# Kernel tuning notes

Hardware: AMD Instinct MI355X
Metric: run time of the kernel (lower is better)

## Reference

```python
import jax, jax.numpy as jnp
import numpy as np

NUM_HEADS = 16


def setup_inputs() -> dict:
    key = jax.random.key(0)
    k1, k2, k3 = jax.random.split(key, 3)
    b, s, d_model = 4, 4096, 1024
    x = jax.random.normal(k1, (b, s, d_model), dtype=jnp.float32)
    w_qkv = jax.random.normal(k2, (3 * d_model, d_model), dtype=jnp.float32) * 0.02
    b_qkv = jnp.zeros((3 * d_model,), dtype=jnp.float32)
    w_out = jax.random.normal(k3, (d_model, d_model), dtype=jnp.float32) * 0.02
    b_out = jnp.zeros((d_model,), dtype=jnp.float32)
    return {"x": x, "w_qkv": w_qkv, "b_qkv": b_qkv, "w_out": w_out, "b_out": b_out}


def reference(x, w_qkv, b_qkv, w_out, b_out):
    b, s, d_model = x.shape
    h = NUM_HEADS
    hd = d_model // h
    # qkv projection: [b, s, 3*d_model]
    qkv = jnp.einsum('bsd,ed->bse', x, w_qkv) + b_qkv
    # rearrange 'b s (three h d) -> three b h s d'
    qkv = qkv.reshape(b, s, 3, h, hd).transpose(2, 0, 3, 1, 4)  # [3, b, h, s, hd]
    q, k, v = qkv[0], qkv[1], qkv[2]
    # elu feature map
    q = jax.nn.elu(q) + 1.0
    k = jax.nn.elu(k) + 1.0
    # kv state: [b, h, hd, hd]
    kv = jnp.einsum('bhsd,bhse->bhde', k, v)
    # output: [b, h, s, hd]
    out = jnp.einsum('bhsd,bhde->bhse', q, kv)
    # normalization (elementwise divide by per-feature k sum, broadcast over s)
    k_sum = k.sum(axis=-2, keepdims=True)  # [b, h, 1, hd]
    out = out / (k_sum + 1e-6)
    # 'b h s d -> b s (h d)'
    out = out.transpose(0, 2, 1, 3).reshape(b, s, d_model)
    return jnp.einsum('bsd,ed->bse', out, w_out) + b_out
```

## Files before the change

### kernel.cpp

```cpp
#include <hip/hip_runtime.h>
#include <stdint.h>

typedef float f32x4 __attribute__((ext_vector_type(4)));
typedef __bf16 bf16x8 __attribute__((ext_vector_type(8)));
typedef unsigned short u16;
typedef u16 u16x8 __attribute__((ext_vector_type(8)));

__device__ __forceinline__ u16 f2bf(float f) {
  uint32_t u = __builtin_bit_cast(uint32_t, f);
  return (u16)((u + 0x7fffu + ((u >> 16) & 1u)) >> 16);
}
__device__ __forceinline__ float bf2f(u16 h) {
  uint32_t u = ((uint32_t)h) << 16;
  return __builtin_bit_cast(float, u);
}
__device__ __forceinline__ float elup1(float x) {
  return x > 0.f ? x + 1.f : __expf(x);
}
__device__ __forceinline__ void gll16(const void* g, void* l) {
  __builtin_amdgcn_global_load_lds(
      (const __attribute__((address_space(1))) unsigned int*)g,
      (__attribute__((address_space(3))) unsigned int*)l, 16, 0, 0);
}

#define BAR() __builtin_amdgcn_s_barrier()
#define VMC(n) asm volatile("s_waitcnt vmcnt(" #n ")" ::: "memory")

__global__ void cvt_all_kernel(const float* __restrict__ x, u16* __restrict__ xb,
                               const float* __restrict__ wq, u16* __restrict__ wqb,
                               const float* __restrict__ wo, u16* __restrict__ wob) {
  int i = blockIdx.x * 256 + threadIdx.x;
  const float* in;
  u16* out;
  if (i < 4194304) {
    in = x; out = xb;
  } else if (i < 4980736) {
    in = wq; out = wqb; i -= 4194304;
  } else {
    in = wo; out = wob; i -= 4980736;
  }
  float4 f = ((const float4*)in)[i];
  ushort4 o;
  o.x = f2bf(f.x); o.y = f2bf(f.y); o.z = f2bf(f.z); o.w = f2bf(f.w);
  ((ushort4*)out)[i] = o;
}

template <int EPI>
__global__ __launch_bounds__(512, 2)
void gemm256(const u16* __restrict__ A, int lda, const u16* __restrict__ B,
             const float* __restrict__ bias, void* __restrict__ Cout,
             int N, int K, int nbj, int bstep) {
  __shared__ __align__(16) u16 lds[65536];
  const int tid = threadIdx.x;
  const int wave = tid >> 6, lane = tid & 63;
  const int fr = lane & 15, fq = lane >> 4;
  const int wm = wave >> 2, wn = wave & 3;

  const int nwg = gridDim.x;
  const int cpx = nwg >> 3;
  const int swz = (blockIdx.x & 7) * cpx + (blockIdx.x >> 3);
  const int bi = swz / nbj, bj = swz % nbj;

  const u16* Ab = A + (size_t)bi * 256 * lda;
  const u16* Bb = B + (size_t)(bi >> 4) * bstep + (size_t)bj * 256 * K;

  const int l8 = lane >> 3;
  const int cswz = ((lane & 7) ^ l8) << 3;
  const int r6 = wave * 8 + l8;

#define STAGE_A(d, h, k0)                                                      \
  { _Pragma("unroll")                                                          \
    for (int i_ = 0; i_ < 2; ++i_) {                                           \
      int gr_ = i_ * 128 + (h) * 64 + r6;                                      \
      gll16(Ab + (size_t)gr_ * lda + (k0) + cswz,                              \
            &lds[((d) * 32768 + (h) * 16384 + i_ * 8192 + wave * 1024) >> 1]); \
    } }

#define STAGE_B(d, h, k0)                                                      \
  { _Pragma("unroll")                                                          \
    for (int i_ = 0; i_ < 2; ++i_) {                                           \
      int r_ = i_ * 64 + r6;                                                   \
      int gr_ = (r_ >> 5) * 64 + (h) * 32 + (r_ & 31);                         \
      gll16(Bb + (size_t)gr_ * K + (k0) + cswz,                                \
            &lds[(65536 + (d) * 32768 + (h) * 16384 + i_ * 8192 + wave * 1024) >> 1]); \
    } }

#define STAGE_ALL(d, k0) \
  { STAGE_A(d, 0, k0); STAGE_A(d, 1, k0); STAGE_B(d, 0, k0); STAGE_B(d, 1, k0); }

  const int xorc = (fr & 7) << 4;
  const int acol[2] = {(fq * 16) ^ xorc, (64 + fq * 16) ^ xorc};
  const int arow = (wm * 64 + fr) * 128;
  const int brow = (wn * 32 + fr) * 128;

#define LDSV(off) (*(const bf16x8*)&lds[(off) >> 1])

  f32x4 acc[8][4] = {};
  bf16x8 af0[4][2], af1[4][2];
  bf16x8 bfr[2][2][2];

#define READ_A(d, mh, dst)                                                     \
  { _Pragma("unroll")                                                          \
    for (int ks = 0; ks < 2; ++ks) {                                           \
      _Pragma("unroll")                                                        \
      for (int mm = 0; mm < 4; ++mm)                                           \
        dst[mm][ks] = LDSV((d) * 32768 + (mh) * 16384 + arow + mm * 2048 + acol[ks]); \
    } }

#define READ_B(d, nh)                                                          \
  { _Pragma("unroll")                                                          \
    for (int ks = 0; ks < 2; ++ks) {                                           \
      _Pragma("unroll")                                                        \
      for (int nn = 0; nn < 2; ++nn)                                           \
        bfr[nh][nn][ks] = LDSV(65536 + (d) * 32768 + (nh) * 16384 + brow + nn * 2048 + acol[ks]); \
    } }

#define MFMA_Q(mh, nh, src)                                                    \
  { __builtin_amdgcn_s_setprio(1);                                             \
    _Pragma("unroll")                                                          \
    for (int ks = 0; ks < 2; ++ks) {                                           \
      _Pragma("unroll")                                                        \
      for (int mm = 0; mm < 4; ++mm) {                                         \
        _Pragma("unroll")                                                      \
        for (int nn = 0; nn < 2; ++nn)                                         \
          acc[(mh) * 4 + mm][(nh) * 2 + nn] = __builtin_amdgcn_mfma_f32_16x16x32_bf16( \
              src[mm][ks], bfr[nh][nn][ks], acc[(mh) * 4 + mm][(nh) * 2 + nn], 0, 0, 0); \
      } }                                                                      \
    __builtin_amdgcn_s_setprio(0); }

#define TILE_BODY(F, S, afF, afS, d, t)                                        \
  {                                                                            \
    READ_B(d, 0); READ_B(d, 1); READ_A(d, F, afF);                             \
    MFMA_Q(F, 0, afF);                                                         \
    READ_A(d, S, afS);                                                         \
    MFMA_Q(F, 1, afF);                                                         \
    if ((t) + 1 < NT) STAGE_ALL((d) ^ 1, ((t) + 1) << 6);                      \
    MFMA_Q(S, 1, afS);                                                         \
    MFMA_Q(S, 0, afS);                                                         \
  }

  const int NT = K >> 6;
  STAGE_ALL(0, 0);
  VMC(0);
  BAR();

  if ((wave & 1) == 0) {
    for (int t = 0; t < NT; ++t) {
      const int d = t & 1;
      TILE_BODY(0, 1, af0, af1, d, t);
      VMC(0); BAR();
    }
  } else {
    for (int t = 0; t < NT; ++t) {
      const int d = t & 1;
      TILE_BODY(1, 0, af1, af0, d, t);
      VMC(0); BAR();
    }
  }

  const int wrow = wm * 128, wcol = wn * 64;
  if (EPI == 0) {
    const bool do_elu = (bj * 256) < 2048;
    float bv[4];
#pragma unroll
    for (int n = 0; n < 4; ++n) bv[n] = bias[bj * 256 + wcol + n * 16 + fr];
    u16* wbuf = &lds[wave * 8192];
    const int lrow = lane >> 3, lcol = (lane & 7) * 8;
#pragma unroll
    for (int ch = 0; ch < 2; ++ch) {
#pragma unroll
      for (int m2 = 0; m2 < 4; ++m2)
#pragma unroll
        for (int n = 0; n < 4; ++n)
#pragma unroll
          for (int r = 0; r < 4; ++r) {
            float v = acc[ch * 4 + m2][n][r] + bv[n];
            if (do_elu) v = elup1(v);
            wbuf[(m2 * 16 + fq * 4 + r) * 72 + n * 16 + fr] = f2bf(v);
          }
#pragma unroll
      for (int i = 0; i < 8; ++i) {
        bf16x8 val = *(const bf16x8*)&wbuf[(i * 8 + lrow) * 72 + lcol];
        const int rowg = bi * 256 + wrow + ch * 64 + i * 8 + lrow;
        *(bf16x8*)&((u16*)Cout)[(size_t)rowg * N + bj * 256 + wcol + lcol] = val;
      }
    }
  } else {
#pragma unroll
    for (int n = 0; n < 4; ++n) {
      const int colg = bj * 256 + wcol + n * 16 + fr;
      const float bv = bias[colg];
#pragma unroll
      for (int m = 0; m < 8; ++m)
#pragma unroll
        for (int r = 0; r < 4; ++r) {
          const int rowg = bi * 256 + wrow + m * 16 + fq * 4 + r;
          ((float*)Cout)[(size_t)rowg * N + colg] = acc[m][n][r] + bv;
        }
    }
  }
#undef STAGE_A
#undef STAGE_B
#undef STAGE_ALL
#undef READ_A
#undef READ_B
#undef MFMA_Q
#undef TILE_BODY
#undef LDSV
}

__global__ __launch_bounds__(256)
void kv_state_kernel(const u16* __restrict__ qkv, float* __restrict__ pkv,
                     float* __restrict__ pks) {
  const int bh = blockIdx.x, chunk = blockIdx.y;
  const int b = bh >> 4, h = bh & 15;
  const int t = threadIdx.x;
  __shared__ float sK[16][68];
  __shared__ float sV[16][68];
  const int dg = (t & 15) * 4;
  const int eg = (t >> 4) * 4;
  f32x4 acc0 = {}, acc1 = {}, acc2 = {}, acc3 = {};
  f32x4 ak4 = {};
  const size_t rowbase = ((size_t)b * 4096 + (size_t)chunk * 512) * 3072;
  const u16* kp = qkv + rowbase + 1024 + h * 64;
  const u16* vp = qkv + rowbase + 2048 + h * 64;
  const int lhalf = t >> 7, lr = (t >> 3) & 15, lc = (t & 7) * 8;
  const u16* lsrc = lhalf ? vp : kp;
  float* ldst = lhalf ? &sV[lr][lc] : &sK[lr][lc];
  for (int s0 = 0; s0 < 512; s0 += 16) {
    u16x8 v8 = *(const u16x8*)&lsrc[(size_t)(s0 + lr) * 3072 + lc];
#pragma unroll
    for (int j = 0; j < 8; ++j) ldst[j] = bf2f(v8[j]);
    __syncthreads();
#pragma unroll 4
    for (int sl = 0; sl < 16; ++sl) {
      const f32x4 kv4 = *(const f32x4*)&sK[sl][dg];
      const f32x4 vv4 = *(const f32x4*)&sV[sl][eg];
      acc0 += kv4[0] * vv4;
      acc1 += kv4[1] * vv4;
      acc2 += kv4[2] * vv4;
      acc3 += kv4[3] * vv4;
      ak4 += kv4;
    }
    __syncthreads();
  }
  float* outp = pkv + ((size_t)chunk * 64 + bh) * 4096;
  *(f32x4*)&outp[(dg + 0) * 64 + eg] = acc0;
  *(f32x4*)&outp[(dg + 1) * 64 + eg] = acc1;
  *(f32x4*)&outp[(dg + 2) * 64 + eg] = acc2;
  *(f32x4*)&outp[(dg + 3) * 64 + eg] = acc3;
  if (t < 16) *(f32x4*)&pks[((size_t)chunk * 64 + bh) * 64 + dg] = ak4;
}

__global__ __launch_bounds__(256)
void kv_reduce_kernel(const float* __restrict__ pkv, const float* __restrict__ pks,
                      u16* __restrict__ kvnb) {
  const int bh = blockIdx.x;
  const int t = threadIdx.x;
  __shared__ float sks[64];
  if (t < 64) {
    float s = 0.f;
    for (int c = 0; c < 8; ++c) s += pks[((size_t)c * 64 + bh) * 64 + t];
    sks[t] = s + 1e-6f;
  }
  __syncthreads();
#pragma unroll
  for (int j = 0; j < 16; ++j) {
    int idx = t + j * 256;
    float s = 0.f;
    for (int c = 0; c < 8; ++c) s += pkv[((size_t)c * 64 + bh) * 4096 + idx];
    kvnb[(size_t)bh * 4096 + idx] = f2bf(s / sks[idx & 63]);
  }
}

__global__ __launch_bounds__(256)
void w2t_kernel(const u16* __restrict__ wob, const u16* __restrict__ kvnb,
                u16* __restrict__ w2t) {
  const int bh = blockIdx.x;
  const int b = bh >> 4, h = bh & 15;
  const int wave = threadIdx.x >> 6, lane = threadIdx.x & 63;
  const int fr = lane & 15, fq = lane >> 4;
  const int j0 = blockIdx.y * 256 + wave * 64;
  __shared__ u16 sW[4][16 * 72];
  const u16* kvp = kvnb + (size_t)bh * 4096;
  bf16x8 bfr[4][2];
#pragma unroll
  for (int ks = 0; ks < 2; ++ks)
#pragma unroll
    for (int nn = 0; nn < 4; ++nn)
      bfr[nn][ks] = *(const bf16x8*)&kvp[(nn * 16 + fr) * 64 + ks * 32 + fq * 8];
  f32x4 acc[4][4] = {};
#pragma unroll
  for (int mm = 0; mm < 4; ++mm)
#pragma unroll
    for (int ks = 0; ks < 2; ++ks) {
      bf16x8 af = *(const bf16x8*)&wob[(size_t)(j0 + mm * 16 + fr) * 1024 + h * 64 + ks * 32 + fq * 8];
#pragma unroll
      for (int nn = 0; nn < 4; ++nn)
        acc[mm][nn] = __builtin_amdgcn_mfma_f32_16x16x32_bf16(af, bfr[nn][ks], acc[mm][nn], 0, 0, 0);
    }
  u16* wb = &sW[wave][0];
  u16* op = w2t + (size_t)b * 1048576 + h * 64;
  const int lrow = lane >> 3, lcol = (lane & 7) * 8;
#pragma unroll
  for (int mm = 0; mm < 4; ++mm) {
#pragma unroll
    for (int nn = 0; nn < 4; ++nn)
#pragma unroll
      for (int r = 0; r < 4; ++r)
        wb[(fq * 4 + r) * 72 + nn * 16 + fr] = f2bf(acc[mm][nn][r]);
#pragma unroll
    for (int i = 0; i < 2; ++i) {
      bf16x8 val = *(const bf16x8*)&wb[(i * 8 + lrow) * 72 + lcol];
      *(bf16x8*)&op[(size_t)(j0 + mm * 16 + i * 8 + lrow) * 1024 + lcol] = val;
    }
  }
}

extern "C" void kernel_launch(void* const* d_in, const int* in_sizes, int n_in,
                              void* d_out, int out_size, void* d_ws, size_t ws_size,
                              hipStream_t stream) {
  const float* x     = (const float*)d_in[0];
  const float* w_qkv = (const float*)d_in[1];
  const float* b_qkv = (const float*)d_in[2];
  const float* w_out = (const float*)d_in[3];
  const float* b_out = (const float*)d_in[4];
  float* out = (float*)d_out;

  const int M = 16384, Dm = 1024, N3 = 3072;

  char* ws = (char*)d_ws;
  u16* xb     = (u16*)(ws);
  u16* wqb    = (u16*)(ws + 33554432);
  u16* wob    = (u16*)(ws + 39845888);
  u16* qkvb   = (u16*)(ws + 41943040);
  u16* w2t    = (u16*)(ws + 142606336);
  float* pkv  = (float*)(ws + 176160768);
  float* pks  = (float*)(ws + 184549376);
  u16* kvnb   = (u16*)(ws + 184680448);

  cvt_all_kernel<<<20480, 256, 0, stream>>>(x, xb, w_qkv, wqb, w_out, wob);

  gemm256<0><<<(M / 256) * (N3 / 256), 512, 0, stream>>>(
      xb, Dm, wqb, b_qkv, qkvb, N3, Dm, N3 / 256, 0);
  kv_state_kernel<<<dim3(64, 8), 256, 0, stream>>>(qkvb, pkv, pks);
  kv_reduce_kernel<<<64, 256, 0, stream>>>(pkv, pks, kvnb);
  w2t_kernel<<<dim3(64, 4), 256, 0, stream>>>(wob, kvnb, w2t);
  gemm256<1><<<(M / 256) * (Dm / 256), 512, 0, stream>>>(
      qkvb, N3, w2t, b_out, out, Dm, Dm, Dm / 256, 1 << 20);
}
```

Before: 225.0 us.

## Switch GEMM to 32x32x16 MFMA with B loaded directly into registers

Rewrites the 256x256 GEMM main loop to use 32x32x16 bf16 MFMA instructions instead of 16x16x32. B fragments now go straight from global memory into registers, double-buffered across tiles, so only A is staged through LDS, and the LDS allocation is halved. The aim is fewer LDS reads per MFMA, better occupancy, and a simpler schedule. The cost is that B global loads are uncoalesced per-lane 16-byte reads with no LDS reuse across the waves that share columns. The wave-parity scheduling split is also dropped.

```diff
diff --git a/kernel.cpp b/kernel.cpp
--- a/kernel.cpp
+++ b/kernel.cpp
@@ -2,6 +2,7 @@
 #include <stdint.h>
 
 typedef float f32x4 __attribute__((ext_vector_type(4)));
+typedef float f32x16 __attribute__((ext_vector_type(16)));
 typedef __bf16 bf16x8 __attribute__((ext_vector_type(8)));
 typedef unsigned short u16;
 typedef u16 u16x8 __attribute__((ext_vector_type(8)));
@@ -50,11 +51,11 @@
 void gemm256(const u16* __restrict__ A, int lda, const u16* __restrict__ B,
              const float* __restrict__ bias, void* __restrict__ Cout,
              int N, int K, int nbj, int bstep) {
-  __shared__ __align__(16) u16 lds[65536];
+  __shared__ __align__(16) u16 lds[32768];
   const int tid = threadIdx.x;
   const int wave = tid >> 6, lane = tid & 63;
-  const int fr = lane & 15, fq = lane >> 4;
   const int wm = wave >> 2, wn = wave & 3;
+  const int l31 = lane & 31, l5 = lane >> 5;
 
   const int nwg = gridDim.x;
   const int cpx = nwg >> 3;
@@ -63,150 +64,116 @@
 
   const u16* Ab = A + (size_t)bi * 256 * lda;
   const u16* Bb = B + (size_t)(bi >> 4) * bstep + (size_t)bj * 256 * K;
+  const u16* Brow = Bb + (size_t)(wn * 64 + l31) * K;
 
   const int l8 = lane >> 3;
   const int cswz = ((lane & 7) ^ l8) << 3;
   const int r6 = wave * 8 + l8;
 
-#define STAGE_A(d, h, k0)                                                      \
+#define STAGE_A(d, k0)                                                         \
   { _Pragma("unroll")                                                          \
-    for (int i_ = 0; i_ < 2; ++i_) {                                           \
-      int gr_ = i_ * 128 + (h) * 64 + r6;                                      \
-      gll16(Ab + (size_t)gr_ * lda + (k0) + cswz,                              \
-            &lds[((d) * 32768 + (h) * 16384 + i_ * 8192 + wave * 1024) >> 1]); \
-    } }
-
-#define STAGE_B(d, h, k0)                                                      \
+    for (int i_ = 0; i_ < 4; ++i_)                                             \
+      gll16(Ab + (size_t)(i_ * 64 + r6) * lda + (k0) + cswz,                   \
+            &lds[((d) * 32768 + i_ * 8192 + wave * 1024) >> 1]); }
+
+  const int arowb = (wm * 128 + l31) * 128;
+  const int sx = lane & 7;
+
+  f32x16 acc[4][2] = {};
+  bf16x8 af[4];
+  bf16x8 bfA[2][4], bfB[2][4];
+
+#define LOADB(dst, k0)                                                         \
   { _Pragma("unroll")                                                          \
-    for (int i_ = 0; i_ < 2; ++i_) {                                           \
-      int r_ = i_ * 64 + r6;                                                   \
-      int gr_ = (r_ >> 5) * 64 + (h) * 32 + (r_ & 31);                         \
-      gll16(Bb + (size_t)gr_ * K + (k0) + cswz,                                \
-            &lds[(65536 + (d) * 32768 + (h) * 16384 + i_ * 8192 + wave * 1024) >> 1]); \
-    } }
-
-#define STAGE_ALL(d, k0) \
-  { STAGE_A(d, 0, k0); STAGE_A(d, 1, k0); STAGE_B(d, 0, k0); STAGE_B(d, 1, k0); }
-
-  const int xorc = (fr & 7) << 4;
-  const int acol[2] = {(fq * 16) ^ xorc, (64 + fq * 16) ^ xorc};
-  const int arow = (wm * 64 + fr) * 128;
-  const int brow = (wn * 32 + fr) * 128;
-
-#define LDSV(off) (*(const bf16x8*)&lds[(off) >> 1])
-
-  f32x4 acc[8][4] = {};
-  bf16x8 af0[4][2], af1[4][2];
-  bf16x8 bfr[2][2][2];
-
-#define READ_A(d, mh, dst)                                                     \
-  { _Pragma("unroll")                                                          \
-    for (int ks = 0; ks < 2; ++ks) {                                           \
-      _Pragma("unroll")                                                        \
-      for (int mm = 0; mm < 4; ++mm)                                           \
-        dst[mm][ks] = LDSV((d) * 32768 + (mh) * 16384 + arow + mm * 2048 + acol[ks]); \
-    } }
-
-#define READ_B(d, nh)                                                          \
-  { _Pragma("unroll")                                                          \
-    for (int ks = 0; ks < 2; ++ks) {                                           \
+    for (int ks = 0; ks < 4; ++ks) {                                           \
       _Pragma("unroll")                                                        \
       for (int nn = 0; nn < 2; ++nn)                                           \
-        bfr[nh][nn][ks] = LDSV(65536 + (d) * 32768 + (nh) * 16384 + brow + nn * 2048 + acol[ks]); \
+        dst[nn][ks] = *(const bf16x8*)&Brow[(size_t)nn * 32 * K + (k0) + ks * 16 + l5 * 8]; \
     } }
 
-#define MFMA_Q(mh, nh, src)                                                    \
+#define READ_AF(d, ks)                                                         \
+  { _Pragma("unroll")                                                          \
+    for (int mm = 0; mm < 4; ++mm) {                                           \
+      const int slot_ = (((ks) * 2 + l5) ^ sx) << 4;                           \
+      af[mm] = *(const bf16x8*)&lds[((d) * 32768 + arowb + mm * 4096 + slot_) >> 1]; \
+    } }
+
+#define MFMA8(cur, ks)                                                         \
   { __builtin_amdgcn_s_setprio(1);                                             \
     _Pragma("unroll")                                                          \
-    for (int ks = 0; ks < 2; ++ks) {                                           \
+    for (int mm = 0; mm < 4; ++mm) {                                           \
       _Pragma("unroll")                                                        \
-      for (int mm = 0; mm < 4; ++mm) {                                         \
-        _Pragma("unroll")                                                      \
-        for (int nn = 0; nn < 2; ++nn)                                         \
-          acc[(mh) * 4 + mm][(nh) * 2 + nn] = __builtin_amdgcn_mfma_f32_16x16x32_bf16( \
-              src[mm][ks], bfr[nh][nn][ks], acc[(mh) * 4 + mm][(nh) * 2 + nn], 0, 0, 0); \
-      } }                                                                      \
+      for (int nn = 0; nn < 2; ++nn)                                           \
+        acc[mm][nn] = __builtin_amdgcn_mfma_f32_32x32x16_bf16(                 \
+            af[mm], cur[nn][ks], acc[mm][nn], 0, 0, 0);                        \
+    }                                                                          \
     __builtin_amdgcn_s_setprio(0); }
 
-#define TILE_BODY(F, S, afF, afS, d, t)                                        \
+#define TILE(d, cur, nxt, t)                                                   \
   {                                                                            \
-    READ_B(d, 0); READ_B(d, 1); READ_A(d, F, afF);                             \
-    MFMA_Q(F, 0, afF);                                                         \
-    READ_A(d, S, afS);                                                         \
-    MFMA_Q(F, 1, afF);                                                         \
-    if ((t) + 1 < NT) STAGE_ALL((d) ^ 1, ((t) + 1) << 6);                      \
-    MFMA_Q(S, 1, afS);                                                         \
-    MFMA_Q(S, 0, afS);                                                         \
+    if ((t) + 1 < NT) { LOADB(nxt, ((t) + 1) << 6); STAGE_A((d) ^ 1, ((t) + 1) << 6); } \
+    _Pragma("unroll")                                                          \
+    for (int ks = 0; ks < 4; ++ks) { READ_AF(d, ks); MFMA8(cur, ks); }         \
+    VMC(0);                                                                    \
+    BAR();                                                                     \
   }
 
   const int NT = K >> 6;
-  STAGE_ALL(0, 0);
-  VMC(0);
+  STAGE_A(0, 0);
+  LOADB(bfA, 0);
+  VMC(8);
   BAR();
 
-  if ((wave & 1) == 0) {
-    for (int t = 0; t < NT; ++t) {
-      const int d = t & 1;
-      TILE_BODY(0, 1, af0, af1, d, t);
-      VMC(0); BAR();
-    }
-  } else {
-    for (int t = 0; t < NT; ++t) {
-      const int d = t & 1;
-      TILE_BODY(1, 0, af1, af0, d, t);
-      VMC(0); BAR();
-    }
-  }
-
-  const int wrow = wm * 128, wcol = wn * 64;
+  for (int tt = 0; tt < NT; tt += 2) {
+    TILE(0, bfA, bfB, tt);
+    TILE(1, bfB, bfA, tt + 1);
+  }
+
   if (EPI == 0) {
     const bool do_elu = (bj * 256) < 2048;
-    float bv[4];
-#pragma unroll
-    for (int n = 0; n < 4; ++n) bv[n] = bias[bj * 256 + wcol + n * 16 + fr];
-    u16* wbuf = &lds[wave * 8192];
-    const int lrow = lane >> 3, lcol = (lane & 7) * 8;
-#pragma unroll
-    for (int ch = 0; ch < 2; ++ch) {
-#pragma unroll
-      for (int m2 = 0; m2 < 4; ++m2)
-#pragma unroll
-        for (int n = 0; n < 4; ++n)
-#pragma unroll
-          for (int r = 0; r < 4; ++r) {
-            float v = acc[ch * 4 + m2][n][r] + bv[n];
-            if (do_elu) v = elup1(v);
-            wbuf[(m2 * 16 + fq * 4 + r) * 72 + n * 16 + fr] = f2bf(v);
-          }
-#pragma unroll
-      for (int i = 0; i < 8; ++i) {
-        bf16x8 val = *(const bf16x8*)&wbuf[(i * 8 + lrow) * 72 + lcol];
-        const int rowg = bi * 256 + wrow + ch * 64 + i * 8 + lrow;
-        *(bf16x8*)&((u16*)Cout)[(size_t)rowg * N + bj * 256 + wcol + lcol] = val;
+    float bv[2];
+#pragma unroll
+    for (int nn = 0; nn < 2; ++nn) bv[nn] = bias[bj * 256 + wn * 64 + nn * 32 + l31];
+    u16* wbuf = &lds[wave * 2304];
+#pragma unroll
+    for (int mm = 0; mm < 4; ++mm) {
+#pragma unroll
+      for (int nn = 0; nn < 2; ++nn)
+#pragma unroll
+        for (int reg = 0; reg < 16; ++reg) {
+          const int row32 = (reg & 3) + 8 * (reg >> 2) + 4 * l5;
+          float v = acc[mm][nn][reg] + bv[nn];
+          if (do_elu) v = elup1(v);
+          wbuf[row32 * 72 + nn * 32 + l31] = f2bf(v);
+        }
+#pragma unroll
+      for (int i_ = 0; i_ < 4; ++i_) {
+        bf16x8 val = *(const bf16x8*)&wbuf[(i_ * 8 + l8) * 72 + (lane & 7) * 8];
+        const int rowg = bi * 256 + wm * 128 + mm * 32 + i_ * 8 + l8;
+        *(bf16x8*)&((u16*)Cout)[(size_t)rowg * N + bj * 256 + wn * 64 + (lane & 7) * 8] = val;
       }
     }
   } else {
-#pragma unroll
-    for (int n = 0; n < 4; ++n) {
-      const int colg = bj * 256 + wcol + n * 16 + fr;
-      const float bv = bias[colg];
-#pragma unroll
-      for (int m = 0; m < 8; ++m)
-#pragma unroll
-        for (int r = 0; r < 4; ++r) {
-          const int rowg = bi * 256 + wrow + m * 16 + fq * 4 + r;
-          ((float*)Cout)[(size_t)rowg * N + colg] = acc[m][n][r] + bv;
+    float bv[2];
+#pragma unroll
+    for (int nn = 0; nn < 2; ++nn) bv[nn] = bias[bj * 256 + wn * 64 + nn * 32 + l31];
+#pragma unroll
+    for (int mm = 0; mm < 4; ++mm)
+#pragma unroll
+      for (int nn = 0; nn < 2; ++nn) {
+        const int colg = bj * 256 + wn * 64 + nn * 32 + l31;
+#pragma unroll
+        for (int reg = 0; reg < 16; ++reg) {
+          const int rowg = bi * 256 + wm * 128 + mm * 32 + (reg & 3) + 8 * (reg >> 2) + 4 * l5;
+          ((float*)Cout)[(size_t)rowg * N + colg] = acc[mm][nn][reg] + bv[nn];
         }
-    }
+      }
   }
 #undef STAGE_A
-#undef STAGE_B
-#undef STAGE_ALL
-#undef READ_A
-#undef READ_B
-#undef MFMA_Q
-#undef TILE_BODY
-#undef LDSV
+#undef LOADB
+#undef READ_AF
+#undef MFMA8
+#undef TILE
 }
 
 __global__ __launch_bounds__(256)
```

New measurement: 284.0 us. 26.2% more time.

## Restructure GEMM main loop into fine-grained 8-phase barrier-synchronized pipeline

Applied to the files above, without the earlier changes.

Replaces the per-tile ping-pong loop (two wave-parity variants, two A-fragment register sets, one full-tile prefetch per iteration) with a loop unrolled by two tiles. Each iteration has eight phases, and each phase interleaves an LDS fragment read, a staged global-to-LDS load of one quarter-tile, and one MFMA quadrant, with explicit lgkmcnt/vmcnt waits and barriers. The aim is to keep global loads continuously in flight and overlap LDS reads with MFMA, in the style of HipKittens 8-wave schedules, while halving A-fragment register use. It adds many barriers per tile and an odd tail path. It also assumes NT is even and at least 2; the peeled tail does handle the final two tiles.

```diff
diff --git a/kernel.cpp b/kernel.cpp
--- a/kernel.cpp
+++ b/kernel.cpp
@@ -25,6 +25,8 @@
 
 #define BAR() __builtin_amdgcn_s_barrier()
 #define VMC(n) asm volatile("s_waitcnt vmcnt(" #n ")" ::: "memory")
+#define LG0() asm volatile("s_waitcnt lgkmcnt(0)" ::: "memory")
+#define LG8() asm volatile("s_waitcnt lgkmcnt(8)" ::: "memory")
 
 __global__ void cvt_all_kernel(const float* __restrict__ x, u16* __restrict__ xb,
                                const float* __restrict__ wq, u16* __restrict__ wqb,
@@ -85,9 +87,6 @@
             &lds[(65536 + (d) * 32768 + (h) * 16384 + i_ * 8192 + wave * 1024) >> 1]); \
     } }
 
-#define STAGE_ALL(d, k0) \
-  { STAGE_A(d, 0, k0); STAGE_A(d, 1, k0); STAGE_B(d, 0, k0); STAGE_B(d, 1, k0); }
-
   const int xorc = (fr & 7) << 4;
   const int acol[2] = {(fq * 16) ^ xorc, (64 + fq * 16) ^ xorc};
   const int arow = (wm * 64 + fr) * 128;
@@ -96,15 +95,15 @@
 #define LDSV(off) (*(const bf16x8*)&lds[(off) >> 1])
 
   f32x4 acc[8][4] = {};
-  bf16x8 af0[4][2], af1[4][2];
+  bf16x8 af[4][2];
   bf16x8 bfr[2][2][2];
 
-#define READ_A(d, mh, dst)                                                     \
+#define READ_A(d, mh)                                                          \
   { _Pragma("unroll")                                                          \
     for (int ks = 0; ks < 2; ++ks) {                                           \
       _Pragma("unroll")                                                        \
       for (int mm = 0; mm < 4; ++mm)                                           \
-        dst[mm][ks] = LDSV((d) * 32768 + (mh) * 16384 + arow + mm * 2048 + acol[ks]); \
+        af[mm][ks] = LDSV((d) * 32768 + (mh) * 16384 + arow + mm * 2048 + acol[ks]); \
     } }
 
 #define READ_B(d, nh)                                                          \
@@ -115,7 +114,7 @@
         bfr[nh][nn][ks] = LDSV(65536 + (d) * 32768 + (nh) * 16384 + brow + nn * 2048 + acol[ks]); \
     } }
 
-#define MFMA_Q(mh, nh, src)                                                    \
+#define MFMA_Q(mh, nh)                                                         \
   { __builtin_amdgcn_s_setprio(1);                                             \
     _Pragma("unroll")                                                          \
     for (int ks = 0; ks < 2; ++ks) {                                           \
@@ -124,38 +123,54 @@
         _Pragma("unroll")                                                      \
         for (int nn = 0; nn < 2; ++nn)                                         \
           acc[(mh) * 4 + mm][(nh) * 2 + nn] = __builtin_amdgcn_mfma_f32_16x16x32_bf16( \
-              src[mm][ks], bfr[nh][nn][ks], acc[(mh) * 4 + mm][(nh) * 2 + nn], 0, 0, 0); \
+              af[mm][ks], bfr[nh][nn][ks], acc[(mh) * 4 + mm][(nh) * 2 + nn], 0, 0, 0); \
       } }                                                                      \
     __builtin_amdgcn_s_setprio(0); }
 
-#define TILE_BODY(F, S, afF, afS, d, t)                                        \
-  {                                                                            \
-    READ_B(d, 0); READ_B(d, 1); READ_A(d, F, afF);                             \
-    MFMA_Q(F, 0, afF);                                                         \
-    READ_A(d, S, afS);                                                         \
-    MFMA_Q(F, 1, afF);                                                         \
-    if ((t) + 1 < NT) STAGE_ALL((d) ^ 1, ((t) + 1) << 6);                      \
-    MFMA_Q(S, 1, afS);                                                         \
-    MFMA_Q(S, 0, afS);                                                         \
-  }
-
   const int NT = K >> 6;
-  STAGE_ALL(0, 0);
-  VMC(0);
+
+  STAGE_A(0, 0, 0); STAGE_B(0, 0, 0); STAGE_B(0, 1, 0); STAGE_A(0, 1, 0);
+  STAGE_A(1, 0, 64); STAGE_B(1, 0, 64); STAGE_B(1, 1, 64);
+  VMC(6);
   BAR();
 
-  if ((wave & 1) == 0) {
-    for (int t = 0; t < NT; ++t) {
-      const int d = t & 1;
-      TILE_BODY(0, 1, af0, af1, d, t);
-      VMC(0); BAR();
-    }
-  } else {
-    for (int t = 0; t < NT; ++t) {
-      const int d = t & 1;
-      TILE_BODY(1, 0, af1, af0, d, t);
-      VMC(0); BAR();
-    }
+  for (int u = 0; u + 3 < NT; u += 2) {
+    const int k1 = (u + 1) << 6, k2 = (u + 2) << 6, k3 = (u + 3) << 6;
+    READ_A(0, 0); READ_B(0, 0); STAGE_A(1, 1, k1);
+    LG8(); BAR(); LG0(); MFMA_Q(0, 0); BAR();
+    READ_B(0, 1); STAGE_A(0, 0, k2);
+    BAR(); LG0(); MFMA_Q(0, 1); BAR();
+    READ_A(0, 1); STAGE_B(0, 0, k2);
+    BAR(); LG0(); MFMA_Q(1, 1); BAR();
+    STAGE_B(0, 1, k2); VMC(6);
+    BAR(); MFMA_Q(1, 0); BAR();
+    READ_A(1, 0); READ_B(1, 0); STAGE_A(0, 1, k2);
+    LG8(); BAR(); LG0(); MFMA_Q(0, 0); BAR();
+    READ_B(1, 1); STAGE_A(1, 0, k3);
+    BAR(); LG0(); MFMA_Q(0, 1); BAR();
+    READ_A(1, 1); STAGE_B(1, 0, k3);
+    BAR(); LG0(); MFMA_Q(1, 1); BAR();
+    STAGE_B(1, 1, k3); VMC(6);
+    BAR(); MFMA_Q(1, 0); BAR();
+  }
+
+  {
+    const int k1 = (NT - 1) << 6;
+    READ_A(0, 0); READ_B(0, 0); STAGE_A(1, 1, k1);
+    LG8(); BAR(); LG0(); MFMA_Q(0, 0); BAR();
+    READ_B(0, 1);
+    BAR(); LG0(); MFMA_Q(0, 1); BAR();
+    READ_A(0, 1);
+    BAR(); LG0(); MFMA_Q(1, 1); BAR();
+    VMC(0);
+    BAR(); MFMA_Q(1, 0); BAR();
+    READ_A(1, 0); READ_B(1, 0);
+    LG8(); BAR(); LG0(); MFMA_Q(0, 0); BAR();
+    READ_B(1, 1);
+    BAR(); LG0(); MFMA_Q(0, 1); BAR();
+    READ_A(1, 1);
+    BAR(); LG0(); MFMA_Q(1, 1); BAR();
+    MFMA_Q(1, 0); BAR();
   }
 
   const int wrow = wm * 128, wcol = wn * 64;
@@ -201,11 +216,9 @@
   }
 #undef STAGE_A
 #undef STAGE_B
-#undef STAGE_ALL
 #undef READ_A
 #undef READ_B
 #undef MFMA_Q
-#undef TILE_BODY
 #undef LDSV
 }
 
```

New measurement: 253.3 us. 1.13x slower.

## Fuse kv reduction into w2t kernel and double kv_state tile per sync

Applied to the files above, without the earlier changes.

Merges the kv partial-sum reduction and the W_out·kv product into one kernel: the normalized kv block stays in shared memory instead of going through a global buffer, and one launch is removed. Each fused block now loops over all four output column groups, so the grid shrinks from 256 to 64 blocks. Separately, kv_state stages 32 sequence rows per barrier instead of 16, halving the number of syncs. The fused kernel has less parallelism, and each block reduces once and then computes four times as much as before.

```diff
diff --git a/kernel.cpp b/kernel.cpp
--- a/kernel.cpp
+++ b/kernel.cpp
@@ -215,8 +215,8 @@
   const int bh = blockIdx.x, chunk = blockIdx.y;
   const int b = bh >> 4, h = bh & 15;
   const int t = threadIdx.x;
-  __shared__ float sK[16][68];
-  __shared__ float sV[16][68];
+  __shared__ float sK[32][68];
+  __shared__ float sV[32][68];
   const int dg = (t & 15) * 4;
   const int eg = (t >> 4) * 4;
   f32x4 acc0 = {}, acc1 = {}, acc2 = {}, acc3 = {};
@@ -227,13 +227,16 @@
   const int lhalf = t >> 7, lr = (t >> 3) & 15, lc = (t & 7) * 8;
   const u16* lsrc = lhalf ? vp : kp;
   float* ldst = lhalf ? &sV[lr][lc] : &sK[lr][lc];
-  for (int s0 = 0; s0 < 512; s0 += 16) {
-    u16x8 v8 = *(const u16x8*)&lsrc[(size_t)(s0 + lr) * 3072 + lc];
-#pragma unroll
-    for (int j = 0; j < 8; ++j) ldst[j] = bf2f(v8[j]);
+  for (int s0 = 0; s0 < 512; s0 += 32) {
+    u16x8 v8a = *(const u16x8*)&lsrc[(size_t)(s0 + lr) * 3072 + lc];
+    u16x8 v8b = *(const u16x8*)&lsrc[(size_t)(s0 + 16 + lr) * 3072 + lc];
+#pragma unroll
+    for (int j = 0; j < 8; ++j) ldst[j] = bf2f(v8a[j]);
+#pragma unroll
+    for (int j = 0; j < 8; ++j) ldst[16 * 68 + j] = bf2f(v8b[j]);
     __syncthreads();
 #pragma unroll 4
-    for (int sl = 0; sl < 16; ++sl) {
+    for (int sl = 0; sl < 32; ++sl) {
       const f32x4 kv4 = *(const f32x4*)&sK[sl][dg];
       const f32x4 vv4 = *(const f32x4*)&sV[sl][eg];
       acc0 += kv4[0] * vv4;
@@ -253,11 +256,13 @@
 }
 
 __global__ __launch_bounds__(256)
-void kv_reduce_kernel(const float* __restrict__ pkv, const float* __restrict__ pks,
-                      u16* __restrict__ kvnb) {
-  const int bh = blockIdx.x;
+void kvw2t_kernel(const float* __restrict__ pkv, const float* __restrict__ pks,
+                  const u16* __restrict__ wob, u16* __restrict__ w2t) {
+  const int bh = blockIdx.x, b = bh >> 4, h = bh & 15;
   const int t = threadIdx.x;
+  __shared__ u16 skv[64][72];
   __shared__ float sks[64];
+  __shared__ u16 sW[4][16 * 72];
   if (t < 64) {
     float s = 0.f;
     for (int c = 0; c < 8; ++c) s += pks[((size_t)c * 64 + bh) * 64 + t];
@@ -266,53 +271,46 @@
   __syncthreads();
 #pragma unroll
   for (int j = 0; j < 16; ++j) {
-    int idx = t + j * 256;
+    const int idx = t + j * 256;
     float s = 0.f;
     for (int c = 0; c < 8; ++c) s += pkv[((size_t)c * 64 + bh) * 4096 + idx];
-    kvnb[(size_t)bh * 4096 + idx] = f2bf(s / sks[idx & 63]);
-  }
-}
-
-__global__ __launch_bounds__(256)
-void w2t_kernel(const u16* __restrict__ wob, const u16* __restrict__ kvnb,
-                u16* __restrict__ w2t) {
-  const int bh = blockIdx.x;
-  const int b = bh >> 4, h = bh & 15;
-  const int wave = threadIdx.x >> 6, lane = threadIdx.x & 63;
+    skv[idx >> 6][idx & 63] = f2bf(s / sks[idx & 63]);
+  }
+  __syncthreads();
+  const int wave = t >> 6, lane = t & 63;
   const int fr = lane & 15, fq = lane >> 4;
-  const int j0 = blockIdx.y * 256 + wave * 64;
-  __shared__ u16 sW[4][16 * 72];
-  const u16* kvp = kvnb + (size_t)bh * 4096;
   bf16x8 bfr[4][2];
 #pragma unroll
   for (int ks = 0; ks < 2; ++ks)
 #pragma unroll
     for (int nn = 0; nn < 4; ++nn)
-      bfr[nn][ks] = *(const bf16x8*)&kvp[(nn * 16 + fr) * 64 + ks * 32 + fq * 8];
-  f32x4 acc[4][4] = {};
-#pragma unroll
-  for (int mm = 0; mm < 4; ++mm)
-#pragma unroll
-    for (int ks = 0; ks < 2; ++ks) {
-      bf16x8 af = *(const bf16x8*)&wob[(size_t)(j0 + mm * 16 + fr) * 1024 + h * 64 + ks * 32 + fq * 8];
-#pragma unroll
-      for (int nn = 0; nn < 4; ++nn)
-        acc[mm][nn] = __builtin_amdgcn_mfma_f32_16x16x32_bf16(af, bfr[nn][ks], acc[mm][nn], 0, 0, 0);
-    }
+      bfr[nn][ks] = *(const bf16x8*)&skv[nn * 16 + fr][ks * 32 + fq * 8];
   u16* wb = &sW[wave][0];
   u16* op = w2t + (size_t)b * 1048576 + h * 64;
   const int lrow = lane >> 3, lcol = (lane & 7) * 8;
 #pragma unroll
-  for (int mm = 0; mm < 4; ++mm) {
-#pragma unroll
-    for (int nn = 0; nn < 4; ++nn)
-#pragma unroll
-      for (int r = 0; r < 4; ++r)
-        wb[(fq * 4 + r) * 72 + nn * 16 + fr] = f2bf(acc[mm][nn][r]);
-#pragma unroll
-    for (int i = 0; i < 2; ++i) {
-      bf16x8 val = *(const bf16x8*)&wb[(i * 8 + lrow) * 72 + lcol];
-      *(bf16x8*)&op[(size_t)(j0 + mm * 16 + i * 8 + lrow) * 1024 + lcol] = val;
+  for (int st = 0; st < 4; ++st) {
+    const int j0 = st * 256 + wave * 64;
+#pragma unroll
+    for (int mm = 0; mm < 4; ++mm) {
+      f32x4 acc[4] = {};
+#pragma unroll
+      for (int ks = 0; ks < 2; ++ks) {
+        bf16x8 af = *(const bf16x8*)&wob[(size_t)(j0 + mm * 16 + fr) * 1024 + h * 64 + ks * 32 + fq * 8];
+#pragma unroll
+        for (int nn = 0; nn < 4; ++nn)
+          acc[nn] = __builtin_amdgcn_mfma_f32_16x16x32_bf16(af, bfr[nn][ks], acc[nn], 0, 0, 0);
+      }
+#pragma unroll
+      for (int nn = 0; nn < 4; ++nn)
+#pragma unroll
+        for (int r = 0; r < 4; ++r)
+          wb[(fq * 4 + r) * 72 + nn * 16 + fr] = f2bf(acc[nn][r]);
+#pragma unroll
+      for (int i = 0; i < 2; ++i) {
+        bf16x8 val = *(const bf16x8*)&wb[(i * 8 + lrow) * 72 + lcol];
+        *(bf16x8*)&op[(size_t)(j0 + mm * 16 + i * 8 + lrow) * 1024 + lcol] = val;
+      }
     }
   }
 }
@@ -337,15 +335,13 @@
   u16* w2t    = (u16*)(ws + 142606336);
   float* pkv  = (float*)(ws + 176160768);
   float* pks  = (float*)(ws + 184549376);
-  u16* kvnb   = (u16*)(ws + 184680448);
 
   cvt_all_kernel<<<20480, 256, 0, stream>>>(x, xb, w_qkv, wqb, w_out, wob);
 
   gemm256<0><<<(M / 256) * (N3 / 256), 512, 0, stream>>>(
       xb, Dm, wqb, b_qkv, qkvb, N3, Dm, N3 / 256, 0);
   kv_state_kernel<<<dim3(64, 8), 256, 0, stream>>>(qkvb, pkv, pks);
-  kv_reduce_kernel<<<64, 256, 0, stream>>>(pkv, pks, kvnb);
-  w2t_kernel<<<dim3(64, 4), 256, 0, stream>>>(wob, kvnb, w2t);
+  kvw2t_kernel<<<64, 256, 0, stream>>>(pkv, pks, wob, w2t);
   gemm256<1><<<(M / 256) * (Dm / 256), 512, 0, stream>>>(
       qkvb, N3, w2t, b_out, out, Dm, Dm, Dm / 256, 1 << 20);
 }
```

Result: no change. 221.8 us (-1.4%).
